# Kernel tuning notes

Hardware: AMD Instinct MI355X
Metric: run time of the kernel (lower is better)

## Reference

```python
import jax, jax.numpy as jnp
import numpy as np

B, T, IN, H, HD, OUT = 8192, 24, 3, 16, 32, 3


def _linear(x, w, b):
    return x @ w.T + b


def _gru_cell(x, h, wih, whh, bih, bhh):
    # torch nn.GRU single-layer cell, gate order (r, z, n)
    gi = x @ wih.T + bih
    gh = h @ whh.T + bhh
    ir, iz, ic = jnp.split(gi, 3, axis=-1)
    hr, hz, hc = jnp.split(gh, 3, axis=-1)
    r = jax.nn.sigmoid(ir + hr)
    z = jax.nn.sigmoid(iz + hz)
    n = jnp.tanh(ic + r * hc)
    return (1.0 - z) * n + z * h


def setup_inputs() -> dict:
    key = jax.random.key(0)
    ks = iter(jax.random.split(key, 40))

    def p(shp, s=0.1):
        return jax.random.normal(next(ks), shp, jnp.float32) * s

    return {
        "x": jax.random.normal(next(ks), (B, T, IN), jnp.float32),
        "h0_enc": p((B, H), 0.2),   # stands in for xavier_normal_ h_0 of encoder
        "h0_dec": p((B, HD), 0.2),  # stands in for xavier_normal_ h_0 of decoder
        "attn1_w": p((IN, H)), "attn1_b": p((IN,)),
        "attn2_w": p((IN, IN)), "attn2_b": p((IN,)),
        "attn3_w": p((IN, IN)), "attn3_b": p((IN,)),
        "enc_wih": p((3 * H, IN)), "enc_whh": p((3 * H, H)),
        "enc_bih": p((3 * H,)), "enc_bhh": p((3 * H,)),
        "l1_w": p((HD, HD)), "l1_b": p((HD,)),
        "l2_w": p((HD, H)), "l2_b": p((HD,)),
        "l3_w": p((1, HD)), "l3_b": p((1,)),
        "l4_w": p((HD, H + IN)), "l4_b": p((HD,)),
        "dec_wih": p((3 * HD, HD)), "dec_whh": p((3 * HD, HD)),
        "dec_bih": p((3 * HD,)), "dec_bhh": p((3 * HD,)),
        "fc_w": p((OUT, HD)), "fc_b": p((OUT,)),
    }


def reference(x, h0_enc, h0_dec, attn1_w, attn1_b, attn2_w, attn2_b, attn3_w, attn3_b,
              enc_wih, enc_whh, enc_bih, enc_bhh,
              l1_w, l1_b, l2_w, l2_b, l3_w, l3_b, l4_w, l4_b,
              dec_wih, dec_whh, dec_bih, dec_bhh, fc_w, fc_b):
    xt = x.transpose(1, 0, 2)  # (T, B, IN)

    # ---- Encoder: input-attention + GRU, scanned over T ----
    def enc_step(h, x_s):
        w1 = _linear(h, attn1_w, attn1_b)            # (B, IN)
        w2 = _linear(x_s, attn2_w, attn2_b)          # (B, IN)
        v = _linear(jnp.tanh(w1 + w2), attn3_w, attn3_b)
        alpha = jax.nn.softmax(v, axis=1)            # over input features
        wx = x_s * alpha
        hn = _gru_cell(wx, h, enc_wih, enc_whh, enc_bih, enc_bhh)
        return hn, hn

    _, enc_seq = jax.lax.scan(enc_step, h0_enc, xt)  # (T, B, H)
    enc = enc_seq.transpose(1, 0, 2)                 # (B, T, H)

    # ---- Decoder: temporal attention over encoder states + GRU ----
    w2d = _linear(enc, l2_w, l2_b)                   # (B, T, HD); loop-invariant

    def dec_step(h, x_s):
        w1 = _linear(h, l1_w, l1_b)                                        # (B, HD)
        a = _linear(jnp.tanh(w1[:, None, :] + w2d), l3_w, l3_b)[..., 0]    # (B, T)
        wa = jax.nn.softmax(a, axis=1)
        wc = jnp.einsum('bth,bt->bh', enc, wa)                             # (B, H)
        y0 = _linear(jnp.concatenate([wc, x_s], axis=1), l4_w, l4_b)       # (B, HD)
        hn = _gru_cell(y0, h, dec_wih, dec_whh, dec_bih, dec_bhh)
        return hn, hn

    _, dec_seq = jax.lax.scan(dec_step, h0_dec, xt)  # (T, B, HD)
    return _linear(dec_seq[-1], fc_w, fc_b)          # (B, OUT)
```

## Files before the change

### kernel.cpp

```cpp
#include <hip/hip_runtime.h>

#define NB 8192
#define NT 24

typedef float v2f __attribute__((ext_vector_type(2)));

__device__ __forceinline__ float rcp_fast(float x) { return __builtin_amdgcn_rcpf(x); }
__device__ __forceinline__ float sigmoid_f(float x) { return rcp_fast(1.f + __expf(-x)); }
__device__ __forceinline__ float tanh_f(float x) { return 1.f - 2.f * rcp_fast(1.f + __expf(2.f * x)); }
__device__ __forceinline__ void creg_fence() { asm volatile("" ::: "memory"); }
__device__ __forceinline__ v2f v2(float a, float b) { v2f r; r.x = a; r.y = b; return r; }
__device__ __forceinline__ v2f v2s(float a) { v2f r; r.x = a; r.y = a; return r; }
__device__ __forceinline__ v2f v2fma(v2f a, v2f b, v2f c) { return __builtin_elementwise_fma(a, b, c); }

__device__ __forceinline__ float dpp16_sum(float x) {
  int v;
  v = __builtin_amdgcn_update_dpp(0, __float_as_int(x), 0xB1, 0xF, 0xF, true);
  x += __int_as_float(v);
  v = __builtin_amdgcn_update_dpp(0, __float_as_int(x), 0x4E, 0xF, 0xF, true);
  x += __int_as_float(v);
  v = __builtin_amdgcn_update_dpp(0, __float_as_int(x), 0x141, 0xF, 0xF, true);
  x += __int_as_float(v);
  v = __builtin_amdgcn_update_dpp(0, __float_as_int(x), 0x140, 0xF, 0xF, true);
  x += __int_as_float(v);
  return x;
}

#define GATE_PK16(T, hq, kk, gr, gz, gn)                        \
  do {                                                          \
    const float4 a0 = T[(0 * 16 + 2 * (kk)) * 16 + jj];         \
    const float4 a1 = T[(0 * 16 + 2 * (kk) + 1) * 16 + jj];     \
    const float4 b0 = T[(1 * 16 + 2 * (kk)) * 16 + jj];         \
    const float4 b1 = T[(1 * 16 + 2 * (kk) + 1) * 16 + jj];     \
    const float4 c0 = T[(2 * 16 + 2 * (kk)) * 16 + jj];         \
    const float4 c1 = T[(2 * 16 + 2 * (kk) + 1) * 16 + jj];     \
    gr = v2fma(v2s(hq.x), v2(a0.x, a0.y), gr);                  \
    gr = v2fma(v2s(hq.y), v2(a0.z, a0.w), gr);                  \
    gr = v2fma(v2s(hq.z), v2(a1.x, a1.y), gr);                  \
    gr = v2fma(v2s(hq.w), v2(a1.z, a1.w), gr);                  \
    gz = v2fma(v2s(hq.x), v2(b0.x, b0.y), gz);                  \
    gz = v2fma(v2s(hq.y), v2(b0.z, b0.w), gz);                  \
    gz = v2fma(v2s(hq.z), v2(b1.x, b1.y), gz);                  \
    gz = v2fma(v2s(hq.w), v2(b1.z, b1.w), gz);                  \
    gn = v2fma(v2s(hq.x), v2(c0.x, c0.y), gn);                  \
    gn = v2fma(v2s(hq.y), v2(c0.z, c0.w), gn);                  \
    gn = v2fma(v2s(hq.z), v2(c1.x, c1.y), gn);                  \
    gn = v2fma(v2s(hq.w), v2(c1.z, c1.w), gn);                  \
  } while (0)

#define GATE_PK8(T, hq, kk, gr, gz, gn)                         \
  do {                                                          \
    const float4 a0 = T[(0 * 8 + 2 * (kk)) * 16 + jj];          \
    const float4 a1 = T[(0 * 8 + 2 * (kk) + 1) * 16 + jj];      \
    const float4 b0 = T[(1 * 8 + 2 * (kk)) * 16 + jj];          \
    const float4 b1 = T[(1 * 8 + 2 * (kk) + 1) * 16 + jj];      \
    const float4 c0 = T[(2 * 8 + 2 * (kk)) * 16 + jj];          \
    const float4 c1 = T[(2 * 8 + 2 * (kk) + 1) * 16 + jj];      \
    gr = v2fma(v2s(hq.x), v2(a0.x, a0.y), gr);                  \
    gr = v2fma(v2s(hq.y), v2(a0.z, a0.w), gr);                  \
    gr = v2fma(v2s(hq.z), v2(a1.x, a1.y), gr);                  \
    gr = v2fma(v2s(hq.w), v2(a1.z, a1.w), gr);                  \
    gz = v2fma(v2s(hq.x), v2(b0.x, b0.y), gz);                  \
    gz = v2fma(v2s(hq.y), v2(b0.z, b0.w), gz);                  \
    gz = v2fma(v2s(hq.z), v2(b1.x, b1.y), gz);                  \
    gz = v2fma(v2s(hq.w), v2(b1.z, b1.w), gz);                  \
    gn = v2fma(v2s(hq.x), v2(c0.x, c0.y), gn);                  \
    gn = v2fma(v2s(hq.y), v2(c0.z, c0.w), gn);                  \
    gn = v2fma(v2s(hq.z), v2(c1.x, c1.y), gn);                  \
    gn = v2fma(v2s(hq.w), v2(c1.z, c1.w), gn);                  \
  } while (0)

__global__ __launch_bounds__(256, 3) void darnn_kernel(
    const float* __restrict__ x, const float* __restrict__ h0_enc, const float* __restrict__ h0_dec,
    const float* __restrict__ attn1_w, const float* __restrict__ attn1_b,
    const float* __restrict__ attn2_w, const float* __restrict__ attn2_b,
    const float* __restrict__ attn3_w, const float* __restrict__ attn3_b,
    const float* __restrict__ enc_wih, const float* __restrict__ enc_whh,
    const float* __restrict__ enc_bih, const float* __restrict__ enc_bhh,
    const float* __restrict__ l1_w, const float* __restrict__ l1_b,
    const float* __restrict__ l2_w, const float* __restrict__ l2_b,
    const float* __restrict__ l3_w, const float* __restrict__ l3_b,
    const float* __restrict__ l4_w, const float* __restrict__ l4_b,
    const float* __restrict__ dec_wih, const float* __restrict__ dec_whh,
    const float* __restrict__ dec_bih, const float* __restrict__ dec_bhh,
    const float* __restrict__ fc_w, const float* __restrict__ fc_b,
    float* __restrict__ out)
{
  __shared__ float4 s_dwhh4[768];
  __shared__ float4 s_l1w4[256];
  __shared__ float4 s_l2w4[128];
  __shared__ float4 s_m4[384];
  __shared__ float4 s_cmx[96];
  __shared__ float4 s_x4[16][24];
  __shared__ float s_bc[16][48];

  const int tid = threadIdx.x;
  const int g = tid >> 4;
  const int jj = tid & 15;
  const int b = blockIdx.x * 16 + g;
  const int j0 = jj, j1 = jj + 16;

  for (int i = tid; i < 768; i += 256) {
    const int q = i >> 8, cp = (i >> 4) & 15, j = i & 15;
    const int r0 = q * 32 + j, r1 = r0 + 16, c0 = 2 * cp;
    float4 f;
    f.x = dec_whh[r0 * 32 + c0]; f.y = dec_whh[r1 * 32 + c0];
    f.z = dec_whh[r0 * 32 + c0 + 1]; f.w = dec_whh[r1 * 32 + c0 + 1];
    s_dwhh4[i] = f;
  }
  {
    const int cp = tid >> 4, j = tid & 15, c0 = 2 * cp;
    float4 f;
    f.x = l1_w[j * 32 + c0]; f.y = l1_w[(j + 16) * 32 + c0];
    f.z = l1_w[j * 32 + c0 + 1]; f.w = l1_w[(j + 16) * 32 + c0 + 1];
    s_l1w4[tid] = f;
  }
  if (tid < 128) {
    const int cp = tid >> 4, j = tid & 15, c0 = 2 * cp;
    float4 e;
    e.x = l2_w[j * 16 + c0]; e.y = l2_w[(j + 16) * 16 + c0];
    e.z = l2_w[j * 16 + c0 + 1]; e.w = l2_w[(j + 16) * 16 + c0 + 1];
    s_l2w4[tid] = e;
  }
  for (int i = tid; i < 384; i += 256) {
    const int j = i & 15, t4 = i >> 4;
    const int q = t4 >> 3, cp = t4 & 7;
    const int r0 = q * 32 + j, r1 = r0 + 16, c0 = 2 * cp, c1 = c0 + 1;
    float4 f; f.x = 0.f; f.y = 0.f; f.z = 0.f; f.w = 0.f;
    for (int k = 0; k < 32; ++k) {
      const float w0 = dec_wih[r0 * 32 + k], w1 = dec_wih[r1 * 32 + k];
      const float lc0 = l4_w[k * 19 + c0], lc1 = l4_w[k * 19 + c1];
      f.x += w0 * lc0; f.y += w1 * lc0; f.z += w0 * lc1; f.w += w1 * lc1;
    }
    s_m4[i] = f;
  }
  for (int r = tid; r < 96; r += 256) {
    float c = dec_bih[r], m0 = 0.f, m1 = 0.f, m2 = 0.f;
    for (int k = 0; k < 32; ++k) {
      const float w = dec_wih[r * 32 + k];
      c += w * l4_b[k];
      m0 += w * l4_w[k * 19 + 16]; m1 += w * l4_w[k * 19 + 17]; m2 += w * l4_w[k * 19 + 18];
    }
    float4 f; f.x = c; f.y = m0; f.z = m1; f.w = m2;
    s_cmx[r] = f;
  }
  {
    const int b0 = blockIdx.x * 16;
    for (int i = tid; i < 16 * 24; i += 256) {
      const int gg = i / 24, tt = i - gg * 24;
      const float* src = x + (b0 + gg) * 72 + tt * 3;
      float4 f; f.x = src[0]; f.y = src[1]; f.z = src[2]; f.w = 0.f;
      s_x4[gg][tt] = f;
    }
  }
  __syncthreads();

  const float A1c0 = attn1_w[jj], A1c1 = attn1_w[16 + jj], A1c2 = attn1_w[32 + jj];
  const float a1b0 = attn1_b[0], a1b1 = attn1_b[1], a1b2 = attn1_b[2];
  float A2[9], A3[9];
#pragma unroll
  for (int i = 0; i < 9; ++i) { A2[i] = attn2_w[i]; A3[i] = attn3_w[i]; }
  const float a2b0 = attn2_b[0], a2b1 = attn2_b[1], a2b2 = attn2_b[2];
  const float a3b0 = attn3_b[0], a3b1 = attn3_b[1], a3b2 = attn3_b[2];
  float WI[3][3];
#pragma unroll
  for (int c = 0; c < 3; ++c)
#pragma unroll
    for (int i = 0; i < 3; ++i) WI[c][i] = enc_wih[(c * 16 + jj) * 3 + i];
  const float BI0 = enc_bih[jj], BI1 = enc_bih[16 + jj], BI2 = enc_bih[32 + jj];
  v2f WHr[8], WHz[8], WHn[8];
#pragma unroll
  for (int k = 0; k < 8; ++k) {
    WHr[k] = v2(enc_whh[jj * 16 + 2 * k], enc_whh[jj * 16 + 2 * k + 1]);
    WHz[k] = v2(enc_whh[(16 + jj) * 16 + 2 * k], enc_whh[(16 + jj) * 16 + 2 * k + 1]);
    WHn[k] = v2(enc_whh[(32 + jj) * 16 + 2 * k], enc_whh[(32 + jj) * 16 + 2 * k + 1]);
  }
  const float BH0 = enc_bhh[jj], BH1 = enc_bhh[16 + jj], BH2 = enc_bhh[32 + jj];
  const v2f l2bv = v2(l2_b[j0], l2_b[j1]);

  float h = h0_enc[b * 16 + jj];
  float enc_reg[NT];
  v2f w2dv[NT];

  s_bc[g][jj] = h;
  creg_fence();

#pragma unroll
  for (int t = 0; t < NT; ++t) {
    const float4 xq = s_x4[g][t];
    const float xs0 = xq.x, xs1 = xq.y, xs2 = xq.z;
    const float w10 = dpp16_sum(h * A1c0) + a1b0;
    const float w11 = dpp16_sum(h * A1c1) + a1b1;
    const float w12 = dpp16_sum(h * A1c2) + a1b2;
    const float w20 = a2b0 + xs0 * A2[0] + xs1 * A2[1] + xs2 * A2[2];
    const float w21 = a2b1 + xs0 * A2[3] + xs1 * A2[4] + xs2 * A2[5];
    const float w22 = a2b2 + xs0 * A2[6] + xs1 * A2[7] + xs2 * A2[8];
    const float t0 = tanh_f(w10 + w20), t1 = tanh_f(w11 + w21), t2 = tanh_f(w12 + w22);
    const float v0 = a3b0 + t0 * A3[0] + t1 * A3[1] + t2 * A3[2];
    const float v1 = a3b1 + t0 * A3[3] + t1 * A3[4] + t2 * A3[5];
    const float v2_ = a3b2 + t0 * A3[6] + t1 * A3[7] + t2 * A3[8];
    const float e0 = __expf(v0), e1 = __expf(v1), e2 = __expf(v2_);
    const float rs = rcp_fast(e0 + e1 + e2);
    const float wx0 = xs0 * e0 * rs, wx1 = xs1 * e1 * rs, wx2 = xs2 * e2 * rs;
    const float gir = BI0 + wx0 * WI[0][0] + wx1 * WI[0][1] + wx2 * WI[0][2];
    const float giz = BI1 + wx0 * WI[1][0] + wx1 * WI[1][1] + wx2 * WI[1][2];
    const float gin = BI2 + wx0 * WI[2][0] + wx1 * WI[2][1] + wx2 * WI[2][2];
    v2f ar = v2s(0.f), az = v2s(0.f), an = v2s(0.f);
#pragma unroll
    for (int kk = 0; kk < 4; ++kk) {
      const float4 hq = *(const float4*)&s_bc[g][4 * kk];
      const v2f hp0 = v2(hq.x, hq.y), hp1 = v2(hq.z, hq.w);
      ar = v2fma(hp0, WHr[2 * kk], ar); ar = v2fma(hp1, WHr[2 * kk + 1], ar);
      az = v2fma(hp0, WHz[2 * kk], az); az = v2fma(hp1, WHz[2 * kk + 1], az);
      an = v2fma(hp0, WHn[2 * kk], an); an = v2fma(hp1, WHn[2 * kk + 1], an);
    }
    const float ghr = BH0 + ar.x + ar.y;
    const float ghz = BH1 + az.x + az.y;
    const float ghn = BH2 + an.x + an.y;
    const float r = sigmoid_f(gir + ghr);
    const float z = sigmoid_f(giz + ghz);
    const float n = tanh_f(gin + r * ghn);
    h = (1.f - z) * n + z * h;
    enc_reg[t] = h;
    s_bc[g][jj] = h;
    creg_fence();
    v2f w2t = l2bv;
#pragma unroll
    for (int kk = 0; kk < 4; ++kk) {
      const float4 hq = *(const float4*)&s_bc[g][4 * kk];
      const float4 f0 = s_l2w4[(2 * kk) * 16 + jj];
      const float4 f1 = s_l2w4[(2 * kk + 1) * 16 + jj];
      w2t = v2fma(v2s(hq.x), v2(f0.x, f0.y), w2t);
      w2t = v2fma(v2s(hq.y), v2(f0.z, f0.w), w2t);
      w2t = v2fma(v2s(hq.z), v2(f1.x, f1.y), w2t);
      w2t = v2fma(v2s(hq.w), v2(f1.z, f1.w), w2t);
    }
    w2dv[t] = w2t;
  }

  const v2f l1bv = v2(l1_b[j0], l1_b[j1]);
  const v2f l3v = v2(l3_w[j0], l3_w[j1]);
  const v2f dhrv = v2(dec_bhh[j0], dec_bhh[j1]);
  const v2f dhzv = v2(dec_bhh[32 + j0], dec_bhh[32 + j1]);
  const v2f dhnv = v2(dec_bhh[64 + j0], dec_bhh[64 + j1]);
  const float4 cr0 = s_cmx[j0], cr1 = s_cmx[j1];
  const float4 cz0 = s_cmx[32 + j0], cz1 = s_cmx[32 + j1];
  const float4 cn0 = s_cmx[64 + j0], cn1 = s_cmx[64 + j1];
  const v2f crc = v2(cr0.x, cr1.x), crx0 = v2(cr0.y, cr1.y), crx1 = v2(cr0.z, cr1.z), crx2 = v2(cr0.w, cr1.w);
  const v2f czc = v2(cz0.x, cz1.x), czx0 = v2(cz0.y, cz1.y), czx1 = v2(cz0.z, cz1.z), czx2 = v2(cz0.w, cz1.w);
  const v2f cnc = v2(cn0.x, cn1.x), cnx0 = v2(cn0.y, cn1.y), cnx1 = v2(cn0.z, cn1.z), cnx2 = v2(cn0.w, cn1.w);

  float hd0 = h0_dec[b * 32 + j0], hd1 = h0_dec[b * 32 + j1];

  for (int t = 0; t < NT; ++t) {
    const float4 xq = s_x4[g][t];

    s_bc[g][jj] = hd0;
    s_bc[g][16 + jj] = hd1;
    creg_fence();

    v2f w1v = l1bv;
    v2f hrv = dhrv, hzv = dhzv, hnv = dhnv;
#pragma unroll
    for (int kk = 0; kk < 8; ++kk) {
      const float4 hq = *(const float4*)&s_bc[g][4 * kk];
      const float4 f0 = s_l1w4[(2 * kk) * 16 + jj];
      const float4 f1 = s_l1w4[(2 * kk + 1) * 16 + jj];
      w1v = v2fma(v2s(hq.x), v2(f0.x, f0.y), w1v);
      w1v = v2fma(v2s(hq.y), v2(f0.z, f0.w), w1v);
      w1v = v2fma(v2s(hq.z), v2(f1.x, f1.y), w1v);
      w1v = v2fma(v2s(hq.w), v2(f1.z, f1.w), w1v);
      GATE_PK16(s_dwhh4, hq, kk, hrv, hzv, hnv);
    }

    float ssum0 = 0.f, ssum1 = 0.f, wca0 = 0.f, wca1 = 0.f;
#pragma unroll
    for (int ch = 0; ch < 6; ++ch) {
      float p[4];
#pragma unroll
      for (int u = 0; u < 4; ++u) {
        const v2f av = w1v + w2dv[4 * ch + u];
        p[u] = __expf(dpp16_sum(l3v.x * tanh_f(av.x) + l3v.y * tanh_f(av.y)));
      }
      ssum0 += p[0] + p[1];
      ssum1 += p[2] + p[3];
      wca0 += p[0] * enc_reg[4 * ch] + p[1] * enc_reg[4 * ch + 1];
      wca1 += p[2] * enc_reg[4 * ch + 2] + p[3] * enc_reg[4 * ch + 3];
    }
    const float wc = (wca0 + wca1) * rcp_fast(ssum0 + ssum1);

    s_bc[g][jj] = wc;
    creg_fence();
    v2f irv = crc, izv = czc, inv = cnc;
    irv = v2fma(v2s(xq.x), crx0, irv); irv = v2fma(v2s(xq.y), crx1, irv); irv = v2fma(v2s(xq.z), crx2, irv);
    izv = v2fma(v2s(xq.x), czx0, izv); izv = v2fma(v2s(xq.y), czx1, izv); izv = v2fma(v2s(xq.z), czx2, izv);
    inv = v2fma(v2s(xq.x), cnx0, inv); inv = v2fma(v2s(xq.y), cnx1, inv); inv = v2fma(v2s(xq.z), cnx2, inv);
#pragma unroll
    for (int kk = 0; kk < 4; ++kk) {
      const float4 cq = *(const float4*)&s_bc[g][4 * kk];
      GATE_PK8(s_m4, cq, kk, irv, izv, inv);
    }

    const float r0 = sigmoid_f(irv.x + hrv.x), r1 = sigmoid_f(irv.y + hrv.y);
    const float z0 = sigmoid_f(izv.x + hzv.x), z1 = sigmoid_f(izv.y + hzv.y);
    const float n0 = tanh_f(inv.x + r0 * hnv.x), n1 = tanh_f(inv.y + r1 * hnv.y);
    hd0 = (1.f - z0) * n0 + z0 * hd0;
    hd1 = (1.f - z1) * n1 + z1 * hd1;
  }

  const float p0 = dpp16_sum(hd0 * fc_w[jj] + hd1 * fc_w[16 + jj]) + fc_b[0];
  const float p1 = dpp16_sum(hd0 * fc_w[32 + jj] + hd1 * fc_w[48 + jj]) + fc_b[1];
  const float p2 = dpp16_sum(hd0 * fc_w[64 + jj] + hd1 * fc_w[80 + jj]) + fc_b[2];
  if (jj == 0) {
    out[b * 3 + 0] = p0;
    out[b * 3 + 1] = p1;
    out[b * 3 + 2] = p2;
  }
}

extern "C" void kernel_launch(void* const* d_in, const int* in_sizes, int n_in,
                              void* d_out, int out_size, void* d_ws, size_t ws_size,
                              hipStream_t stream) {
  const float* p[27];
  for (int i = 0; i < 27; ++i) p[i] = (const float*)d_in[i];
  darnn_kernel<<<NB / 16, 256, 0, stream>>>(
      p[0], p[1], p[2], p[3], p[4], p[5], p[6], p[7], p[8],
      p[9], p[10], p[11], p[12], p[13], p[14], p[15], p[16], p[17], p[18],
      p[19], p[20], p[21], p[22], p[23], p[24], p[25], p[26],
      (float*)d_out);
}
```

Measured before the change: 138.8 us.

## Fold exp2 scaling into weights, share reciprocals, keep decoder input matrix in registers

Pre-scales the attention weights and biases by 2*log2(e) or log2(e) so tanh and softmax can use the raw exp2 instruction without extra multiplies. In the decoder attention it merges the two tanh reciprocals into one, and in the encoder it computes all three tanh values from a single reciprocal. The fused l4/dec_wih matrix moves from LDS into 24 float4 registers per thread, and occupancy hint drops from 3 to 2 blocks to make room. The GRU update is rewritten as n + z*(h-n). Risks are higher register pressure, lower occupancy, and possible overflow or precision loss in the products of (1+exp) terms.

Result: faster. 122.1 us (-12.0%).

```diff
diff --git a/kernel.cpp b/kernel.cpp
--- a/kernel.cpp
+++ b/kernel.cpp
@@ -5,9 +5,13 @@
 
 typedef float v2f __attribute__((ext_vector_type(2)));
 
+#define K2L 2.8853900817779268f
+#define L2E 1.4426950408889634f
+
 __device__ __forceinline__ float rcp_fast(float x) { return __builtin_amdgcn_rcpf(x); }
-__device__ __forceinline__ float sigmoid_f(float x) { return rcp_fast(1.f + __expf(-x)); }
-__device__ __forceinline__ float tanh_f(float x) { return 1.f - 2.f * rcp_fast(1.f + __expf(2.f * x)); }
+__device__ __forceinline__ float exp2_fast(float x) { return __builtin_amdgcn_exp2f(x); }
+__device__ __forceinline__ float sigmoid_f(float x) { return rcp_fast(1.f + exp2_fast(-L2E * x)); }
+__device__ __forceinline__ float tanh_f(float x) { return 1.f - 2.f * rcp_fast(1.f + exp2_fast(K2L * x)); }
 __device__ __forceinline__ void creg_fence() { asm volatile("" ::: "memory"); }
 __device__ __forceinline__ v2f v2(float a, float b) { v2f r; r.x = a; r.y = b; return r; }
 __device__ __forceinline__ v2f v2s(float a) { v2f r; r.x = a; r.y = a; return r; }
@@ -48,14 +52,14 @@
     gn = v2fma(v2s(hq.w), v2(c1.z, c1.w), gn);                  \
   } while (0)
 
-#define GATE_PK8(T, hq, kk, gr, gz, gn)                         \
+#define GATE_PK8R(hq, kk, gr, gz, gn)                           \
   do {                                                          \
-    const float4 a0 = T[(0 * 8 + 2 * (kk)) * 16 + jj];          \
-    const float4 a1 = T[(0 * 8 + 2 * (kk) + 1) * 16 + jj];      \
-    const float4 b0 = T[(1 * 8 + 2 * (kk)) * 16 + jj];          \
-    const float4 b1 = T[(1 * 8 + 2 * (kk) + 1) * 16 + jj];      \
-    const float4 c0 = T[(2 * 8 + 2 * (kk)) * 16 + jj];          \
-    const float4 c1 = T[(2 * 8 + 2 * (kk) + 1) * 16 + jj];      \
+    const float4 a0 = rm[0 * 8 + 2 * (kk)];                     \
+    const float4 a1 = rm[0 * 8 + 2 * (kk) + 1];                 \
+    const float4 b0 = rm[1 * 8 + 2 * (kk)];                     \
+    const float4 b1 = rm[1 * 8 + 2 * (kk) + 1];                 \
+    const float4 c0 = rm[2 * 8 + 2 * (kk)];                     \
+    const float4 c1 = rm[2 * 8 + 2 * (kk) + 1];                 \
     gr = v2fma(v2s(hq.x), v2(a0.x, a0.y), gr);                  \
     gr = v2fma(v2s(hq.y), v2(a0.z, a0.w), gr);                  \
     gr = v2fma(v2s(hq.z), v2(a1.x, a1.y), gr);                  \
@@ -70,7 +74,7 @@
     gn = v2fma(v2s(hq.w), v2(c1.z, c1.w), gn);                  \
   } while (0)
 
-__global__ __launch_bounds__(256, 3) void darnn_kernel(
+__global__ __launch_bounds__(256, 2) void darnn_kernel(
     const float* __restrict__ x, const float* __restrict__ h0_enc, const float* __restrict__ h0_dec,
     const float* __restrict__ attn1_w, const float* __restrict__ attn1_b,
     const float* __restrict__ attn2_w, const float* __restrict__ attn2_b,
@@ -111,15 +115,15 @@
   {
     const int cp = tid >> 4, j = tid & 15, c0 = 2 * cp;
     float4 f;
-    f.x = l1_w[j * 32 + c0]; f.y = l1_w[(j + 16) * 32 + c0];
-    f.z = l1_w[j * 32 + c0 + 1]; f.w = l1_w[(j + 16) * 32 + c0 + 1];
+    f.x = K2L * l1_w[j * 32 + c0]; f.y = K2L * l1_w[(j + 16) * 32 + c0];
+    f.z = K2L * l1_w[j * 32 + c0 + 1]; f.w = K2L * l1_w[(j + 16) * 32 + c0 + 1];
     s_l1w4[tid] = f;
   }
   if (tid < 128) {
     const int cp = tid >> 4, j = tid & 15, c0 = 2 * cp;
     float4 e;
-    e.x = l2_w[j * 16 + c0]; e.y = l2_w[(j + 16) * 16 + c0];
-    e.z = l2_w[j * 16 + c0 + 1]; e.w = l2_w[(j + 16) * 16 + c0 + 1];
+    e.x = K2L * l2_w[j * 16 + c0]; e.y = K2L * l2_w[(j + 16) * 16 + c0];
+    e.z = K2L * l2_w[j * 16 + c0 + 1]; e.w = K2L * l2_w[(j + 16) * 16 + c0 + 1];
     s_l2w4[tid] = e;
   }
   for (int i = tid; i < 384; i += 256) {
@@ -155,13 +159,13 @@
   }
   __syncthreads();
 
-  const float A1c0 = attn1_w[jj], A1c1 = attn1_w[16 + jj], A1c2 = attn1_w[32 + jj];
-  const float a1b0 = attn1_b[0], a1b1 = attn1_b[1], a1b2 = attn1_b[2];
+  const float A1c0 = K2L * attn1_w[jj], A1c1 = K2L * attn1_w[16 + jj], A1c2 = K2L * attn1_w[32 + jj];
+  const float a1b0 = K2L * attn1_b[0], a1b1 = K2L * attn1_b[1], a1b2 = K2L * attn1_b[2];
   float A2[9], A3[9];
 #pragma unroll
-  for (int i = 0; i < 9; ++i) { A2[i] = attn2_w[i]; A3[i] = attn3_w[i]; }
-  const float a2b0 = attn2_b[0], a2b1 = attn2_b[1], a2b2 = attn2_b[2];
-  const float a3b0 = attn3_b[0], a3b1 = attn3_b[1], a3b2 = attn3_b[2];
+  for (int i = 0; i < 9; ++i) { A2[i] = K2L * attn2_w[i]; A3[i] = L2E * attn3_w[i]; }
+  const float a2b0 = K2L * attn2_b[0], a2b1 = K2L * attn2_b[1], a2b2 = K2L * attn2_b[2];
+  const float a3b0 = L2E * attn3_b[0], a3b1 = L2E * attn3_b[1], a3b2 = L2E * attn3_b[2];
   float WI[3][3];
 #pragma unroll
   for (int c = 0; c < 3; ++c)
@@ -176,7 +180,7 @@
     WHn[k] = v2(enc_whh[(32 + jj) * 16 + 2 * k], enc_whh[(32 + jj) * 16 + 2 * k + 1]);
   }
   const float BH0 = enc_bhh[jj], BH1 = enc_bhh[16 + jj], BH2 = enc_bhh[32 + jj];
-  const v2f l2bv = v2(l2_b[j0], l2_b[j1]);
+  const v2f l2bv = v2(K2L * l2_b[j0], K2L * l2_b[j1]);
 
   float h = h0_enc[b * 16 + jj];
   float enc_reg[NT];
@@ -195,11 +199,20 @@
     const float w20 = a2b0 + xs0 * A2[0] + xs1 * A2[1] + xs2 * A2[2];
     const float w21 = a2b1 + xs0 * A2[3] + xs1 * A2[4] + xs2 * A2[5];
     const float w22 = a2b2 + xs0 * A2[6] + xs1 * A2[7] + xs2 * A2[8];
-    const float t0 = tanh_f(w10 + w20), t1 = tanh_f(w11 + w21), t2 = tanh_f(w12 + w22);
+    const float Aa = 1.f + exp2_fast(w10 + w20);
+    const float Ab = 1.f + exp2_fast(w11 + w21);
+    const float Ac = 1.f + exp2_fast(w12 + w22);
+    const float Pab = Aa * Ab;
+    const float r3 = rcp_fast(Pab * Ac);
+    const float tc2 = Pab * r3;
+    const float tAc = Ac * r3;
+    const float ta2 = Ab * tAc;
+    const float tb2 = Aa * tAc;
+    const float t0 = 1.f - 2.f * ta2, t1 = 1.f - 2.f * tb2, t2 = 1.f - 2.f * tc2;
     const float v0 = a3b0 + t0 * A3[0] + t1 * A3[1] + t2 * A3[2];
     const float v1 = a3b1 + t0 * A3[3] + t1 * A3[4] + t2 * A3[5];
     const float v2_ = a3b2 + t0 * A3[6] + t1 * A3[7] + t2 * A3[8];
-    const float e0 = __expf(v0), e1 = __expf(v1), e2 = __expf(v2_);
+    const float e0 = exp2_fast(v0), e1 = exp2_fast(v1), e2 = exp2_fast(v2_);
     const float rs = rcp_fast(e0 + e1 + e2);
     const float wx0 = xs0 * e0 * rs, wx1 = xs1 * e1 * rs, wx2 = xs2 * e2 * rs;
     const float gir = BI0 + wx0 * WI[0][0] + wx1 * WI[0][1] + wx2 * WI[0][2];
@@ -220,7 +233,7 @@
     const float r = sigmoid_f(gir + ghr);
     const float z = sigmoid_f(giz + ghz);
     const float n = tanh_f(gin + r * ghn);
-    h = (1.f - z) * n + z * h;
+    h = n + z * (h - n);
     enc_reg[t] = h;
     s_bc[g][jj] = h;
     creg_fence();
@@ -238,8 +251,12 @@
     w2dv[t] = w2t;
   }
 
-  const v2f l1bv = v2(l1_b[j0], l1_b[j1]);
-  const v2f l3v = v2(l3_w[j0], l3_w[j1]);
+  float4 rm[24];
+#pragma unroll
+  for (int i = 0; i < 24; ++i) rm[i] = s_m4[i * 16 + jj];
+
+  const v2f l1bv = v2(K2L * l1_b[j0], K2L * l1_b[j1]);
+  const v2f m3v = v2(-2.f * L2E * l3_w[j0], -2.f * L2E * l3_w[j1]);
   const v2f dhrv = v2(dec_bhh[j0], dec_bhh[j1]);
   const v2f dhzv = v2(dec_bhh[32 + j0], dec_bhh[32 + j1]);
   const v2f dhnv = v2(dec_bhh[64 + j0], dec_bhh[64 + j1]);
@@ -280,7 +297,12 @@
 #pragma unroll
       for (int u = 0; u < 4; ++u) {
         const v2f av = w1v + w2dv[4 * ch + u];
-        p[u] = __expf(dpp16_sum(l3v.x * tanh_f(av.x) + l3v.y * tanh_f(av.y)));
+        const float Ax = 1.f + exp2_fast(av.x);
+        const float Ay = 1.f + exp2_fast(av.y);
+        const float rr = rcp_fast(Ax * Ay);
+        float uu = m3v.x * Ay;
+        uu = fmaf(m3v.y, Ax, uu);
+        p[u] = exp2_fast(dpp16_sum(uu * rr));
       }
       ssum0 += p[0] + p[1];
       ssum1 += p[2] + p[3];
@@ -298,14 +320,14 @@
 #pragma unroll
     for (int kk = 0; kk < 4; ++kk) {
       const float4 cq = *(const float4*)&s_bc[g][4 * kk];
-      GATE_PK8(s_m4, cq, kk, irv, izv, inv);
+      GATE_PK8R(cq, kk, irv, izv, inv);
     }
 
     const float r0 = sigmoid_f(irv.x + hrv.x), r1 = sigmoid_f(irv.y + hrv.y);
     const float z0 = sigmoid_f(izv.x + hzv.x), z1 = sigmoid_f(izv.y + hzv.y);
     const float n0 = tanh_f(inv.x + r0 * hnv.x), n1 = tanh_f(inv.y + r1 * hnv.y);
-    hd0 = (1.f - z0) * n0 + z0 * hd0;
-    hd1 = (1.f - z1) * n1 + z1 * hd1;
+    hd0 = n0 + z0 * (hd0 - n0);
+    hd1 = n1 + z1 * (hd1 - n1);
   }
 
   const float p0 = dpp16_sum(hd0 * fc_w[jj] + hd1 * fc_w[16 + jj]) + fc_b[0];
```
